# Optimization experiments

Measured on AMD Instinct MI355X. Metric: run time of the kernel, lower is better.

## Reference

```python
import jax, jax.numpy as jnp
import numpy as np

EMBED_DIM = 768
NUM_HEADS = 12
HEAD_DIM = EMBED_DIM // NUM_HEADS
SCALE = HEAD_DIM ** -0.5
EPS = 1e-5


def _layernorm(x, g, b):
    m = jnp.mean(x, axis=-1, keepdims=True)
    v = jnp.mean(jnp.square(x - m), axis=-1, keepdims=True)
    return (x - m) * jax.lax.rsqrt(v + EPS) * g + b


def setup_inputs() -> dict:
    key = jax.random.key(0)
    ks = jax.random.split(key, 8)
    B, N, D, Hd = 16, 1024, EMBED_DIM, HEAD_DIM
    x = jax.random.normal(ks[0], (B, N, D), dtype=jnp.float32)
    W_qkv = jax.random.normal(ks[1], (D, 3 * D), dtype=jnp.float32) * (D ** -0.5)
    b_qkv = jnp.zeros((3 * D,), dtype=jnp.float32)
    W_proj = jax.random.normal(ks[2], (D, D), dtype=jnp.float32) * (D ** -0.5)
    b_proj = jnp.zeros((D,), dtype=jnp.float32)
    return {
        "x": x,
        "ln_g": jnp.ones((D,), jnp.float32), "ln_b": jnp.zeros((D,), jnp.float32),
        "W_qkv": W_qkv, "b_qkv": b_qkv,
        "qn_g": jnp.ones((Hd,), jnp.float32), "qn_b": jnp.zeros((Hd,), jnp.float32),
        "kn_g": jnp.ones((Hd,), jnp.float32), "kn_b": jnp.zeros((Hd,), jnp.float32),
        "W_proj": W_proj, "b_proj": b_proj,
    }


def reference(x, ln_g, ln_b, W_qkv, b_qkv, qn_g, qn_b, kn_g, kn_b, W_proj, b_proj):
    B, N, D = x.shape
    H, Hd = NUM_HEADS, HEAD_DIM
    xn = _layernorm(x, ln_g, ln_b)                      # qkv_norm (pre-LN of embed_dim)
    qkv = xn @ W_qkv + b_qkv                            # [B,N,3D]
    qkv = qkv.reshape(B, N, 3, H, Hd)
    q = jnp.transpose(qkv[:, :, 0], (0, 2, 1, 3))       # [B,H,N,Hd]
    k = jnp.transpose(qkv[:, :, 1], (0, 2, 1, 3))
    v = jnp.transpose(qkv[:, :, 2], (0, 2, 1, 3))
    q = _layernorm(q, qn_g, qn_b)                       # per-head QK LayerNorm
    k = _layernorm(k, kn_g, kn_b)
    attn = jnp.einsum("bhnd,bhmd->bhnm", q, k) * SCALE
    attn = jax.nn.softmax(attn, axis=-1)
    out = jnp.einsum("bhnm,bhmd->bhnd", attn, v)        # [B,H,N,Hd]
    out = jnp.transpose(out, (0, 2, 1, 3)).reshape(B, N, D)
    return out @ W_proj + b_proj
```

## Files before the change

kernel.cpp:

```cpp
#include <hip/hip_runtime.h>

typedef _Float16 half8 __attribute__((ext_vector_type(8)));
typedef _Float16 half4 __attribute__((ext_vector_type(4)));
typedef _Float16 half2v __attribute__((ext_vector_type(2)));
typedef float f32x4 __attribute__((ext_vector_type(4)));

#define B_    16
#define N_    1024
#define D_    768
#define H_    12
#define M_    (B_ * N_)
#define QKVN_ 2304
#define EPS_  1e-5f
#define QS_   0.18033688011112042f

__device__ __forceinline__ float exp2_fast(float x) {
#if __has_builtin(__builtin_amdgcn_exp2f)
    return __builtin_amdgcn_exp2f(x);
#else
    return __builtin_exp2f(x);
#endif
}

__device__ __forceinline__ size_t aidx(int row, int d) {
    return ((size_t)((row >> 8) * 12 + (d >> 6))) * 16384
         + ((((row >> 4) & 15) * 2) + ((d >> 5) & 1)) * 512
         + (((d >> 3) & 3)) * 128 + (row & 15) * 8 + (d & 7);
}

__global__ __launch_bounds__(256) void convert_w(const float* __restrict__ Wqkv,
                                                 const float* __restrict__ Wproj,
                                                 _Float16* __restrict__ wqkv_p,
                                                 _Float16* __restrict__ wproj_p) {
    __shared__ float T[64][65];
    int t = blockIdx.x;
    const float* W; _Float16* O; int NW, k0, n0;
    if (t < 432) { W = Wqkv;  O = wqkv_p;  NW = QKVN_; k0 = (t % 12) * 64; n0 = (t / 12) * 64; }
    else { t -= 432; W = Wproj; O = wproj_p; NW = D_;  k0 = (t % 12) * 64; n0 = (t / 12) * 64; }
    int c = threadIdx.x & 63, r4 = threadIdx.x >> 6;
#pragma unroll
    for (int i = 0; i < 16; ++i) {
        int k = i * 4 + r4;
        T[c][k] = W[(size_t)(k0 + k) * NW + n0 + c];
    }
    __syncthreads();
    int kt = k0 >> 6;
    int ntile = n0 >> 7;
    int t16base = (n0 >> 4) & 7;
#pragma unroll
    for (int it = 0; it < 2; ++it) {
        int g = it * 256 + threadIdx.x;
        int t16l = g >> 7, ksub = (g >> 6) & 1, lgI = (g >> 4) & 3, p = g & 15;
        half8 v;
#pragma unroll
        for (int e = 0; e < 8; ++e)
            v[e] = (_Float16)T[t16l * 16 + p][ksub * 32 + lgI * 8 + e];
        *(half8*)&O[((size_t)(ntile * 12 + kt)) * 8192 +
                    ((t16base + t16l) * 2 + ksub) * 512 + lgI * 128 + p * 8] = v;
    }
}

__global__ __launch_bounds__(256) void ln_embed(const float* __restrict__ x,
                                                const float* __restrict__ g,
                                                const float* __restrict__ bb,
                                                _Float16* __restrict__ xp) {
    int row = blockIdx.x;
    int tid = threadIdx.x;
    const float2* xr = (const float2*)(x + (size_t)row * D_);
    float2 v0 = xr[tid];
    float2 v1 = make_float2(0.f, 0.f);
    if (tid < 128) v1 = xr[256 + tid];
    float s = v0.x + v0.y + v1.x + v1.y;
    float q = v0.x * v0.x + v0.y * v0.y + v1.x * v1.x + v1.y * v1.y;
#pragma unroll
    for (int m = 32; m >= 1; m >>= 1) {
        s += __shfl_xor(s, m);
        q += __shfl_xor(q, m);
    }
    __shared__ float ss[4], qq[4];
    int wave = tid >> 6;
    if ((tid & 63) == 0) { ss[wave] = s; qq[wave] = q; }
    __syncthreads();
    float S = ss[0] + ss[1] + ss[2] + ss[3];
    float Q = qq[0] + qq[1] + qq[2] + qq[3];
    float mean = S * (1.f / 768.f);
    float var  = Q * (1.f / 768.f) - mean * mean;
    float rstd = rsqrtf(var + EPS_);
    const float2* g2 = (const float2*)g;
    const float2* b2 = (const float2*)bb;
    {
        int d0 = 2 * tid;
        float2 ga = g2[tid], ba = b2[tid];
        half2v w;
        w[0] = (_Float16)((v0.x - mean) * rstd * ga.x + ba.x);
        w[1] = (_Float16)((v0.y - mean) * rstd * ga.y + ba.y);
        *(half2v*)&xp[aidx(row, d0)] = w;
    }
    if (tid < 128) {
        int d0 = 512 + 2 * tid;
        float2 ga = g2[256 + tid], ba = b2[256 + tid];
        half2v w;
        w[0] = (_Float16)((v1.x - mean) * rstd * ga.x + ba.x);
        w[1] = (_Float16)((v1.y - mean) * rstd * ga.y + ba.y);
        *(half2v*)&xp[aidx(row, d0)] = w;
    }
}

__global__ __launch_bounds__(256, 3) void gemm_qkv(const _Float16* __restrict__ Xp,
                                                   const _Float16* __restrict__ Wp,
                                                   const float* __restrict__ bias,
                                                   const float* __restrict__ qn_g,
                                                   const float* __restrict__ qn_b,
                                                   const float* __restrict__ kn_g,
                                                   const float* __restrict__ kn_b,
                                                   _Float16* __restrict__ qo,
                                                   _Float16* __restrict__ ko,
                                                   _Float16* __restrict__ vt) {
    int xcd = blockIdx.x & 7, loc = blockIdx.x >> 3;
    int mblk = xcd * 16 + (loc & 15);
    int nb = loc >> 4;
    int tid = threadIdx.x;
    int wid = tid >> 6, lane = tid & 63;
    int wm = wid >> 1, wn = wid & 1;
    int lg = lane >> 4, l15 = lane & 15;
    bool isV = (nb >= 12);

    const _Float16* pw = Wp + (size_t)nb * 98304 + (wn * 4) * 1024 + lane * 8;
    const _Float16* px = Xp + (size_t)(mblk >> 1) * 196608 +
                         ((mblk & 1) * 8 + wm * 4) * 1024 + lane * 8;

    f32x4 acc[4][4] = {};
    half8 xa0[4], wb0[4], xa1[4], wb1[4];
    auto ld = [&](half8 (&xa)[4], half8 (&wb)[4], int t) {
        int kt = t >> 1, ks = t & 1;
        size_t offW = (size_t)kt * 8192 + ks * 512;
        size_t offX = (size_t)kt * 16384 + ks * 512;
#pragma unroll
        for (int i = 0; i < 4; ++i) {
            xa[i] = *(const half8*)(px + i * 1024 + offX);
            wb[i] = *(const half8*)(pw + i * 1024 + offW);
        }
    };
    auto mmQK = [&](half8 (&xa)[4], half8 (&wb)[4]) {
#pragma unroll
        for (int ni = 0; ni < 4; ++ni)
#pragma unroll
            for (int mi = 0; mi < 4; ++mi)
                acc[ni][mi] = __builtin_amdgcn_mfma_f32_16x16x32_f16(wb[ni], xa[mi], acc[ni][mi], 0, 0, 0);
    };
    auto mmV = [&](half8 (&xa)[4], half8 (&wb)[4]) {
#pragma unroll
        for (int mi = 0; mi < 4; ++mi)
#pragma unroll
            for (int ni = 0; ni < 4; ++ni)
                acc[mi][ni] = __builtin_amdgcn_mfma_f32_16x16x32_f16(xa[mi], wb[ni], acc[mi][ni], 0, 0, 0);
    };

    ld(xa0, wb0, 0);
    if (isV) {
        for (int tt = 0; tt < 11; ++tt) {
            ld(xa1, wb1, 2 * tt + 1);
            mmV(xa0, wb0);
            ld(xa0, wb0, 2 * tt + 2);
            mmV(xa1, wb1);
        }
        ld(xa1, wb1, 23);
        mmV(xa0, wb0);
        mmV(xa1, wb1);
    } else {
        for (int tt = 0; tt < 11; ++tt) {
            ld(xa1, wb1, 2 * tt + 1);
            mmQK(xa0, wb0);
            ld(xa0, wb0, 2 * tt + 2);
            mmQK(xa1, wb1);
        }
        ld(xa1, wb1, 23);
        mmQK(xa0, wb0);
        mmQK(xa1, wb1);
    }

    int m0 = mblk * 128;
    int col0 = nb * 128 + wn * 64;

    if (isV) {
        int hcol = (col0 % 768) >> 6;
        float qkvb[4];
#pragma unroll
        for (int ni = 0; ni < 4; ++ni) qkvb[ni] = bias[col0 + ni * 16 + l15];
#pragma unroll
        for (int mi = 0; mi < 4; ++mi) {
            int r0 = m0 + wm * 64 + mi * 16 + lg * 4;
            int bidx = r0 >> 10, pos = r0 & 1023;
            int kvblk = pos >> 5, h = (pos >> 4) & 1, lgR = (pos >> 2) & 3;
            size_t vbase = ((size_t)(bidx * H_ + hcol) * 32 + kvblk) * 4;
#pragma unroll
            for (int ni = 0; ni < 4; ++ni) {
                half4 h4;
#pragma unroll
                for (int j = 0; j < 4; ++j) h4[j] = (_Float16)(acc[mi][ni][j] + qkvb[ni]);
                *(half4*)&vt[(vbase + ni) * 512 + lgR * 128 + l15 * 8 + h * 4] = h4;
            }
        }
    } else {
        int s = col0 / 768;
        int hcol = (col0 % 768) >> 6;
        const float* gg = (s == 0) ? qn_g : kn_g;
        const float* bv = (s == 0) ? qn_b : kn_b;
        _Float16* dst = (s == 0) ? qo : ko;
        float4 g4[4], b4[4], bi4[4];
#pragma unroll
        for (int ni = 0; ni < 4; ++ni) {
            g4[ni]  = *(const float4*)&gg[ni * 16 + lg * 4];
            b4[ni]  = *(const float4*)&bv[ni * 16 + lg * 4];
            bi4[ni] = *(const float4*)&bias[col0 + ni * 16 + lg * 4];
        }
        int posbase = m0 + wm * 64;
        int bidx = posbase >> 10;
        size_t bh0 = (size_t)(bidx * H_ + hcol) * 65536;
        float scl = (s == 0) ? QS_ : 1.0f;
#pragma unroll
        for (int mi = 0; mi < 4; ++mi) {
            float vv[4][4];
            float sm = 0.f, sq = 0.f;
#pragma unroll
            for (int ni = 0; ni < 4; ++ni)
#pragma unroll
                for (int j = 0; j < 4; ++j) {
                    float bvj = (j == 0) ? bi4[ni].x : (j == 1) ? bi4[ni].y : (j == 2) ? bi4[ni].z : bi4[ni].w;
                    float v = acc[ni][mi][j] + bvj;
                    vv[ni][j] = v;
                    sm += v;
                    sq += v * v;
                }
            sm += __shfl_xor(sm, 16); sq += __shfl_xor(sq, 16);
            sm += __shfl_xor(sm, 32); sq += __shfl_xor(sq, 32);
            float mean = sm * (1.f / 64.f);
            float var  = sq * (1.f / 64.f) - mean * mean;
            float rstd = rsqrtf(var + EPS_) * scl;
            float meanb = mean;
            int posL = ((posbase & 1023) + mi * 16);
            size_t obase = bh0 + (size_t)(posL >> 5) * 2048 + ((posL >> 4) & 1) * 1024
                         + l15 * 8 + (lg & 1) * 4;
#pragma unroll
            for (int ni = 0; ni < 4; ++ni) {
                half4 h4;
#pragma unroll
                for (int j = 0; j < 4; ++j) {
                    float gj = (j == 0) ? g4[ni].x : (j == 1) ? g4[ni].y : (j == 2) ? g4[ni].z : g4[ni].w;
                    float bj = (j == 0) ? b4[ni].x : (j == 1) ? b4[ni].y : (j == 2) ? b4[ni].z : b4[ni].w;
                    h4[j] = (_Float16)((vv[ni][j] - meanb) * rstd * gj + bj * scl);
                }
                dst[obase + (ni >> 1) * 512 + (((ni & 1) << 1) | (lg >> 1)) * 128] = h4[0];
                *(half4*)&dst[obase + (ni >> 1) * 512 + (((ni & 1) << 1) | (lg >> 1)) * 128] = h4;
            }
        }
    }
}

struct KV {
    half8 kf[2][2];
    half8 vf[4];
};

__device__ __forceinline__ void ldKV(KV& s, const _Float16* kp, const _Float16* vp, int kvblk) {
    const _Float16* kb = kp + (size_t)kvblk * 2048;
#pragma unroll
    for (int nh = 0; nh < 2; ++nh)
#pragma unroll
        for (int ks = 0; ks < 2; ++ks)
            s.kf[nh][ks] = *(const half8*)(kb + (nh * 2 + ks) * 512);
    const _Float16* vb = vp + (size_t)kvblk * 2048;
#pragma unroll
    for (int di = 0; di < 4; ++di)
        s.vf[di] = *(const half8*)(vb + di * 512);
}

__device__ __forceinline__ void blockKV(const KV& s, const half8 (&qf)[4][2],
                                        f32x4 (&oacc)[4][4], f32x4 (&lacc)[4],
                                        half8 ones) {
#pragma unroll
    for (int mi = 0; mi < 4; ++mi) {
        f32x4 a0 = {}, a1 = {};
#pragma unroll
        for (int ks = 0; ks < 2; ++ks) {
            a0 = __builtin_amdgcn_mfma_f32_16x16x32_f16(s.kf[0][ks], qf[mi][ks], a0, 0, 0, 0);
            a1 = __builtin_amdgcn_mfma_f32_16x16x32_f16(s.kf[1][ks], qf[mi][ks], a1, 0, 0, 0);
        }
        half8 pf;
#pragma unroll
        for (int j = 0; j < 4; ++j) {
            pf[j]     = (_Float16)exp2_fast(a0[j]);
            pf[j + 4] = (_Float16)exp2_fast(a1[j]);
        }
        lacc[mi] = __builtin_amdgcn_mfma_f32_16x16x32_f16(ones, pf, lacc[mi], 0, 0, 0);
#pragma unroll
        for (int di = 0; di < 4; ++di)
            oacc[mi][di] = __builtin_amdgcn_mfma_f32_16x16x32_f16(s.vf[di], pf, oacc[mi][di], 0, 0, 0);
    }
}

__global__ __launch_bounds__(128, 2) void attn(const _Float16* __restrict__ qg,
                                               const _Float16* __restrict__ kg,
                                               const _Float16* __restrict__ vtg,
                                               _Float16* __restrict__ op) {
    int bphys = blockIdx.x;
    int jj = (bphys & 7) * 192 + (bphys >> 3);
    int bh = jj >> 3, qt = jj & 7;
    int b = bh / H_, h = bh % H_;
    int tid = threadIdx.x;
    int wid = tid >> 6, lane = tid & 63;
    int lg = lane >> 4, l15 = lane & 15;
    int qw0 = qt * 128 + wid * 64;

    const _Float16* qp2 = qg + (size_t)bh * 65536 + (size_t)(qw0 >> 5) * 2048 + lane * 8;
    half8 qf[4][2];
#pragma unroll
    for (int mi = 0; mi < 4; ++mi)
#pragma unroll
        for (int ks = 0; ks < 2; ++ks)
            qf[mi][ks] = *(const half8*)(qp2 + (mi >> 1) * 2048 + (mi & 1) * 1024 + ks * 512);

    const _Float16* kp = kg + (size_t)bh * 65536 + lane * 8;
    const _Float16* vp = vtg + (size_t)bh * 65536 + lane * 8;

    half8 ones;
#pragma unroll
    for (int i = 0; i < 8; ++i) ones[i] = (_Float16)1.0f;

    f32x4 oacc[4][4] = {};
    f32x4 lacc[4] = {};

    KV s0, s1;
    ldKV(s0, kp, vp, 0);
    for (int t = 0; t < 16; ++t) {
        ldKV(s1, kp, vp, (2 * t + 1) & 31);
        blockKV(s0, qf, oacc, lacc, ones);
        ldKV(s0, kp, vp, (2 * t + 2) & 31);
        blockKV(s1, qf, oacc, lacc, ones);
    }

#pragma unroll
    for (int mi = 0; mi < 4; ++mi) {
        float inv = 1.f / lacc[mi][0];
        int row0 = b * 1024 + qw0 + mi * 16;
        int mtv = row0 >> 8, t16 = (row0 >> 4) & 15;
#pragma unroll
        for (int di = 0; di < 4; ++di) {
            half4 h4;
#pragma unroll
            for (int j = 0; j < 4; ++j) h4[j] = (_Float16)(oacc[mi][di][j] * inv);
            size_t o = ((size_t)(mtv * 12 + h)) * 16384 + (t16 * 2 + (di >> 1)) * 512
                     + ((di & 1) * 2 + (lg >> 1)) * 128 + l15 * 8 + (lg & 1) * 4;
            *(half4*)&op[o] = h4;
        }
    }
}

__global__ __launch_bounds__(256, 3) void gemm_proj(const _Float16* __restrict__ Ap,
                                                    const _Float16* __restrict__ Wp,
                                                    const float* __restrict__ bias,
                                                    float* __restrict__ out) {
    int xcd = blockIdx.x & 7, loc = blockIdx.x >> 3;
    int mblk = xcd * 16 + (loc & 15);
    int nb = loc >> 4;
    int tid = threadIdx.x;
    int wid = tid >> 6, lane = tid & 63;
    int wm = wid >> 1, wn = wid & 1;
    int lg = lane >> 4, l15 = lane & 15;

    const _Float16* pw = Wp + (size_t)nb * 98304 + (wn * 4) * 1024 + lane * 8;
    const _Float16* px = Ap + (size_t)(mblk >> 1) * 196608 +
                         ((mblk & 1) * 8 + wm * 4) * 1024 + lane * 8;

    f32x4 acc[4][4] = {};
    half8 xa0[4], wb0[4], xa1[4], wb1[4];
    auto ld = [&](half8 (&xa)[4], half8 (&wb)[4], int t) {
        int kt = t >> 1, ks = t & 1;
        size_t offW = (size_t)kt * 8192 + ks * 512;
        size_t offX = (size_t)kt * 16384 + ks * 512;
#pragma unroll
        for (int i = 0; i < 4; ++i) {
            xa[i] = *(const half8*)(px + i * 1024 + offX);
            wb[i] = *(const half8*)(pw + i * 1024 + offW);
        }
    };
    auto mm = [&](half8 (&xa)[4], half8 (&wb)[4]) {
#pragma unroll
        for (int mi = 0; mi < 4; ++mi)
#pragma unroll
            for (int ni = 0; ni < 4; ++ni)
                acc[mi][ni] = __builtin_amdgcn_mfma_f32_16x16x32_f16(xa[mi], wb[ni], acc[mi][ni], 0, 0, 0);
    };
    ld(xa0, wb0, 0);
    for (int tt = 0; tt < 11; ++tt) {
        ld(xa1, wb1, 2 * tt + 1);
        mm(xa0, wb0);
        ld(xa0, wb0, 2 * tt + 2);
        mm(xa1, wb1);
    }
    ld(xa1, wb1, 23);
    mm(xa0, wb0);
    mm(xa1, wb1);

    int m0 = mblk * 128, n0 = nb * 128;
#pragma unroll
    for (int mi = 0; mi < 4; ++mi)
#pragma unroll
        for (int ni = 0; ni < 4; ++ni) {
            int col = n0 + wn * 64 + ni * 16 + l15;
            float bv = bias[col];
#pragma unroll
            for (int j = 0; j < 4; ++j) {
                int row = m0 + wm * 64 + mi * 16 + lg * 4 + j;
                out[(size_t)row * D_ + col] = acc[mi][ni][j] + bv;
            }
        }
}

extern "C" void kernel_launch(void* const* d_in, const int* in_sizes, int n_in,
                              void* d_out, int out_size, void* d_ws, size_t ws_size,
                              hipStream_t stream) {
    const float* x      = (const float*)d_in[0];
    const float* ln_g   = (const float*)d_in[1];
    const float* ln_b   = (const float*)d_in[2];
    const float* W_qkv  = (const float*)d_in[3];
    const float* b_qkv  = (const float*)d_in[4];
    const float* qn_g   = (const float*)d_in[5];
    const float* qn_b   = (const float*)d_in[6];
    const float* kn_g   = (const float*)d_in[7];
    const float* kn_b   = (const float*)d_in[8];
    const float* W_proj = (const float*)d_in[9];
    const float* b_proj = (const float*)d_in[10];
    float* out = (float*)d_out;
    char* ws = (char*)d_ws;

    constexpr size_t XN_SZ    = (size_t)M_ * D_ * 2;
    constexpr size_t WQKVT_SZ = (size_t)QKVN_ * D_ * 2;
    constexpr size_t WPROJT_SZ= (size_t)D_ * D_ * 2;
    constexpr size_t HEAD_SZ  = (size_t)B_ * H_ * N_ * 64 * 2;

    _Float16* xn_p   = (_Float16*)(ws);
    _Float16* wqkv_p = (_Float16*)(ws + XN_SZ);
    _Float16* wproj_p= (_Float16*)(ws + XN_SZ + WQKVT_SZ);
    _Float16* qb     = (_Float16*)(ws + XN_SZ + WQKVT_SZ + WPROJT_SZ);
    _Float16* kb     = (_Float16*)((char*)qb + HEAD_SZ);
    _Float16* vtb    = (_Float16*)((char*)kb + HEAD_SZ);
    _Float16* ao_p   = xn_p;

    convert_w<<<576, 256, 0, stream>>>(W_qkv, W_proj, wqkv_p, wproj_p);
    ln_embed<<<M_, 256, 0, stream>>>(x, ln_g, ln_b, xn_p);
    gemm_qkv<<<(M_ / 128) * (QKVN_ / 128), 256, 0, stream>>>(xn_p, wqkv_p, b_qkv,
                                                             qn_g, qn_b, kn_g, kn_b,
                                                             qb, kb, vtb);
    attn<<<B_ * H_ * (N_ / 128), 128, 0, stream>>>(qb, kb, vtb, ao_p);
    gemm_proj<<<(M_ / 128) * (D_ / 128), 256, 0, stream>>>(ao_p, wproj_p, b_proj, out);
}
```

Before: 190.1 us.

## Split attention KV range across waves and merge prep kernels into one launch

Attention blocks now cover 64 query rows, with each of the two waves processing half of the KV sequence. The partial outputs and row sums are combined through shared memory, which doubles the grid and shortens each wave's serial loop. The weight conversion and embed LayerNorm kernels are merged into a single launch, and a redundant scalar store in the QKV epilogue is removed. The split adds a shared-memory reduction and a barrier, and leaves one wave idle during the epilogue.

```diff
diff --git a/kernel.cpp b/kernel.cpp
--- a/kernel.cpp
+++ b/kernel.cpp
@@ -28,81 +28,84 @@
          + (((d >> 3) & 3)) * 128 + (row & 15) * 8 + (d & 7);
 }
 
-__global__ __launch_bounds__(256) void convert_w(const float* __restrict__ Wqkv,
-                                                 const float* __restrict__ Wproj,
-                                                 _Float16* __restrict__ wqkv_p,
-                                                 _Float16* __restrict__ wproj_p) {
+__global__ __launch_bounds__(256) void prep(const float* __restrict__ x,
+                                            const float* __restrict__ ln_g,
+                                            const float* __restrict__ ln_b,
+                                            const float* __restrict__ Wqkv,
+                                            const float* __restrict__ Wproj,
+                                            _Float16* __restrict__ xp,
+                                            _Float16* __restrict__ wqkv_p,
+                                            _Float16* __restrict__ wproj_p) {
     __shared__ float T[64][65];
-    int t = blockIdx.x;
-    const float* W; _Float16* O; int NW, k0, n0;
-    if (t < 432) { W = Wqkv;  O = wqkv_p;  NW = QKVN_; k0 = (t % 12) * 64; n0 = (t / 12) * 64; }
-    else { t -= 432; W = Wproj; O = wproj_p; NW = D_;  k0 = (t % 12) * 64; n0 = (t / 12) * 64; }
-    int c = threadIdx.x & 63, r4 = threadIdx.x >> 6;
-#pragma unroll
-    for (int i = 0; i < 16; ++i) {
-        int k = i * 4 + r4;
-        T[c][k] = W[(size_t)(k0 + k) * NW + n0 + c];
-    }
-    __syncthreads();
-    int kt = k0 >> 6;
-    int ntile = n0 >> 7;
-    int t16base = (n0 >> 4) & 7;
-#pragma unroll
-    for (int it = 0; it < 2; ++it) {
-        int g = it * 256 + threadIdx.x;
-        int t16l = g >> 7, ksub = (g >> 6) & 1, lgI = (g >> 4) & 3, p = g & 15;
-        half8 v;
-#pragma unroll
-        for (int e = 0; e < 8; ++e)
-            v[e] = (_Float16)T[t16l * 16 + p][ksub * 32 + lgI * 8 + e];
-        *(half8*)&O[((size_t)(ntile * 12 + kt)) * 8192 +
-                    ((t16base + t16l) * 2 + ksub) * 512 + lgI * 128 + p * 8] = v;
-    }
-}
-
-__global__ __launch_bounds__(256) void ln_embed(const float* __restrict__ x,
-                                                const float* __restrict__ g,
-                                                const float* __restrict__ bb,
-                                                _Float16* __restrict__ xp) {
-    int row = blockIdx.x;
-    int tid = threadIdx.x;
-    const float2* xr = (const float2*)(x + (size_t)row * D_);
-    float2 v0 = xr[tid];
-    float2 v1 = make_float2(0.f, 0.f);
-    if (tid < 128) v1 = xr[256 + tid];
-    float s = v0.x + v0.y + v1.x + v1.y;
-    float q = v0.x * v0.x + v0.y * v0.y + v1.x * v1.x + v1.y * v1.y;
-#pragma unroll
-    for (int m = 32; m >= 1; m >>= 1) {
-        s += __shfl_xor(s, m);
-        q += __shfl_xor(q, m);
-    }
-    __shared__ float ss[4], qq[4];
-    int wave = tid >> 6;
-    if ((tid & 63) == 0) { ss[wave] = s; qq[wave] = q; }
-    __syncthreads();
-    float S = ss[0] + ss[1] + ss[2] + ss[3];
-    float Q = qq[0] + qq[1] + qq[2] + qq[3];
-    float mean = S * (1.f / 768.f);
-    float var  = Q * (1.f / 768.f) - mean * mean;
-    float rstd = rsqrtf(var + EPS_);
-    const float2* g2 = (const float2*)g;
-    const float2* b2 = (const float2*)bb;
-    {
-        int d0 = 2 * tid;
-        float2 ga = g2[tid], ba = b2[tid];
-        half2v w;
-        w[0] = (_Float16)((v0.x - mean) * rstd * ga.x + ba.x);
-        w[1] = (_Float16)((v0.y - mean) * rstd * ga.y + ba.y);
-        *(half2v*)&xp[aidx(row, d0)] = w;
-    }
-    if (tid < 128) {
-        int d0 = 512 + 2 * tid;
-        float2 ga = g2[256 + tid], ba = b2[256 + tid];
-        half2v w;
-        w[0] = (_Float16)((v1.x - mean) * rstd * ga.x + ba.x);
-        w[1] = (_Float16)((v1.y - mean) * rstd * ga.y + ba.y);
-        *(half2v*)&xp[aidx(row, d0)] = w;
+    int tb = blockIdx.x;
+    if (tb < 576) {
+        int t = tb;
+        const float* W; _Float16* O; int NW, k0, n0;
+        if (t < 432) { W = Wqkv;  O = wqkv_p;  NW = QKVN_; k0 = (t % 12) * 64; n0 = (t / 12) * 64; }
+        else { t -= 432; W = Wproj; O = wproj_p; NW = D_;  k0 = (t % 12) * 64; n0 = (t / 12) * 64; }
+        int c = threadIdx.x & 63, r4 = threadIdx.x >> 6;
+#pragma unroll
+        for (int i = 0; i < 16; ++i) {
+            int k = i * 4 + r4;
+            T[c][k] = W[(size_t)(k0 + k) * NW + n0 + c];
+        }
+        __syncthreads();
+        int kt = k0 >> 6;
+        int ntile = n0 >> 7;
+        int t16base = (n0 >> 4) & 7;
+#pragma unroll
+        for (int it = 0; it < 2; ++it) {
+            int g = it * 256 + threadIdx.x;
+            int t16l = g >> 7, ksub = (g >> 6) & 1, lgI = (g >> 4) & 3, p = g & 15;
+            half8 v;
+#pragma unroll
+            for (int e = 0; e < 8; ++e)
+                v[e] = (_Float16)T[t16l * 16 + p][ksub * 32 + lgI * 8 + e];
+            *(half8*)&O[((size_t)(ntile * 12 + kt)) * 8192 +
+                        ((t16base + t16l) * 2 + ksub) * 512 + lgI * 128 + p * 8] = v;
+        }
+    } else {
+        int row = tb - 576;
+        int tid = threadIdx.x;
+        const float2* xr = (const float2*)(x + (size_t)row * D_);
+        float2 v0 = xr[tid];
+        float2 v1 = make_float2(0.f, 0.f);
+        if (tid < 128) v1 = xr[256 + tid];
+        float s = v0.x + v0.y + v1.x + v1.y;
+        float q = v0.x * v0.x + v0.y * v0.y + v1.x * v1.x + v1.y * v1.y;
+#pragma unroll
+        for (int m = 32; m >= 1; m >>= 1) {
+            s += __shfl_xor(s, m);
+            q += __shfl_xor(q, m);
+        }
+        float* ss = &T[0][0];
+        float* qq = &T[0][8];
+        int wave = tid >> 6;
+        if ((tid & 63) == 0) { ss[wave] = s; qq[wave] = q; }
+        __syncthreads();
+        float S = ss[0] + ss[1] + ss[2] + ss[3];
+        float Q = qq[0] + qq[1] + qq[2] + qq[3];
+        float mean = S * (1.f / 768.f);
+        float var  = Q * (1.f / 768.f) - mean * mean;
+        float rstd = rsqrtf(var + EPS_);
+        const float2* g2 = (const float2*)ln_g;
+        const float2* b2 = (const float2*)ln_b;
+        {
+            int d0 = 2 * tid;
+            float2 ga = g2[tid], ba = b2[tid];
+            half2v w;
+            w[0] = (_Float16)((v0.x - mean) * rstd * ga.x + ba.x);
+            w[1] = (_Float16)((v0.y - mean) * rstd * ga.y + ba.y);
+            *(half2v*)&xp[aidx(row, d0)] = w;
+        }
+        if (tid < 128) {
+            int d0 = 512 + 2 * tid;
+            float2 ga = g2[256 + tid], ba = b2[256 + tid];
+            half2v w;
+            w[0] = (_Float16)((v1.x - mean) * rstd * ga.x + ba.x);
+            w[1] = (_Float16)((v1.y - mean) * rstd * ga.y + ba.y);
+            *(half2v*)&xp[aidx(row, d0)] = w;
+        }
     }
 }
 
@@ -237,7 +240,6 @@
             float mean = sm * (1.f / 64.f);
             float var  = sq * (1.f / 64.f) - mean * mean;
             float rstd = rsqrtf(var + EPS_) * scl;
-            float meanb = mean;
             int posL = ((posbase & 1023) + mi * 16);
             size_t obase = bh0 + (size_t)(posL >> 5) * 2048 + ((posL >> 4) & 1) * 1024
                          + l15 * 8 + (lg & 1) * 4;
@@ -248,9 +250,8 @@
                 for (int j = 0; j < 4; ++j) {
                     float gj = (j == 0) ? g4[ni].x : (j == 1) ? g4[ni].y : (j == 2) ? g4[ni].z : g4[ni].w;
                     float bj = (j == 0) ? b4[ni].x : (j == 1) ? b4[ni].y : (j == 2) ? b4[ni].z : b4[ni].w;
-                    h4[j] = (_Float16)((vv[ni][j] - meanb) * rstd * gj + bj * scl);
+                    h4[j] = (_Float16)((vv[ni][j] - mean) * rstd * gj + bj * scl);
                 }
-                dst[obase + (ni >> 1) * 512 + (((ni & 1) << 1) | (lg >> 1)) * 128] = h4[0];
                 *(half4*)&dst[obase + (ni >> 1) * 512 + (((ni & 1) << 1) | (lg >> 1)) * 128] = h4;
             }
         }
@@ -303,14 +304,16 @@
                                                const _Float16* __restrict__ kg,
                                                const _Float16* __restrict__ vtg,
                                                _Float16* __restrict__ op) {
+    __shared__ float OB[4][4][4][4][16];
+    __shared__ float LB[4][16];
     int bphys = blockIdx.x;
-    int jj = (bphys & 7) * 192 + (bphys >> 3);
-    int bh = jj >> 3, qt = jj & 7;
+    int jj = (bphys & 7) * 384 + (bphys >> 3);
+    int bh = jj >> 4, qgi = jj & 15;
     int b = bh / H_, h = bh % H_;
     int tid = threadIdx.x;
     int wid = tid >> 6, lane = tid & 63;
     int lg = lane >> 4, l15 = lane & 15;
-    int qw0 = qt * 128 + wid * 64;
+    int qw0 = qgi * 64;
 
     const _Float16* qp2 = qg + (size_t)bh * 65536 + (size_t)(qw0 >> 5) * 2048 + lane * 8;
     half8 qf[4][2];
@@ -322,6 +325,7 @@
 
     const _Float16* kp = kg + (size_t)bh * 65536 + lane * 8;
     const _Float16* vp = vtg + (size_t)bh * 65536 + lane * 8;
+    int kvbase = wid * 16;
 
     half8 ones;
 #pragma unroll
@@ -331,27 +335,42 @@
     f32x4 lacc[4] = {};
 
     KV s0, s1;
-    ldKV(s0, kp, vp, 0);
-    for (int t = 0; t < 16; ++t) {
-        ldKV(s1, kp, vp, (2 * t + 1) & 31);
+    ldKV(s0, kp, vp, kvbase);
+    for (int t = 0; t < 8; ++t) {
+        ldKV(s1, kp, vp, kvbase + ((2 * t + 1) & 15));
         blockKV(s0, qf, oacc, lacc, ones);
-        ldKV(s0, kp, vp, (2 * t + 2) & 31);
+        ldKV(s0, kp, vp, kvbase + ((2 * t + 2) & 15));
         blockKV(s1, qf, oacc, lacc, ones);
     }
 
-#pragma unroll
-    for (int mi = 0; mi < 4; ++mi) {
-        float inv = 1.f / lacc[mi][0];
-        int row0 = b * 1024 + qw0 + mi * 16;
-        int mtv = row0 >> 8, t16 = (row0 >> 4) & 15;
-#pragma unroll
-        for (int di = 0; di < 4; ++di) {
-            half4 h4;
-#pragma unroll
-            for (int j = 0; j < 4; ++j) h4[j] = (_Float16)(oacc[mi][di][j] * inv);
-            size_t o = ((size_t)(mtv * 12 + h)) * 16384 + (t16 * 2 + (di >> 1)) * 512
-                     + ((di & 1) * 2 + (lg >> 1)) * 128 + l15 * 8 + (lg & 1) * 4;
-            *(half4*)&op[o] = h4;
+    if (wid == 1) {
+#pragma unroll
+        for (int mi = 0; mi < 4; ++mi) {
+#pragma unroll
+            for (int di = 0; di < 4; ++di)
+#pragma unroll
+                for (int j = 0; j < 4; ++j)
+                    OB[mi][di][j][lg][l15] = oacc[mi][di][j];
+            if (lg == 0) LB[mi][l15] = lacc[mi][0];
+        }
+    }
+    __syncthreads();
+    if (wid == 0) {
+#pragma unroll
+        for (int mi = 0; mi < 4; ++mi) {
+            float inv = 1.f / (lacc[mi][0] + LB[mi][l15]);
+            int row0 = b * 1024 + qw0 + mi * 16;
+            int mtv = row0 >> 8, t16 = (row0 >> 4) & 15;
+#pragma unroll
+            for (int di = 0; di < 4; ++di) {
+                half4 h4;
+#pragma unroll
+                for (int j = 0; j < 4; ++j)
+                    h4[j] = (_Float16)((oacc[mi][di][j] + OB[mi][di][j][lg][l15]) * inv);
+                size_t o = ((size_t)(mtv * 12 + h)) * 16384 + (t16 * 2 + (di >> 1)) * 512
+                         + ((di & 1) * 2 + (lg >> 1)) * 128 + l15 * 8 + (lg & 1) * 4;
+                *(half4*)&op[o] = h4;
+            }
         }
     }
 }
@@ -447,11 +466,11 @@
     _Float16* vtb    = (_Float16*)((char*)kb + HEAD_SZ);
     _Float16* ao_p   = xn_p;
 
-    convert_w<<<576, 256, 0, stream>>>(W_qkv, W_proj, wqkv_p, wproj_p);
-    ln_embed<<<M_, 256, 0, stream>>>(x, ln_g, ln_b, xn_p);
+    prep<<<576 + M_, 256, 0, stream>>>(x, ln_g, ln_b, W_qkv, W_proj,
+                                       xn_p, wqkv_p, wproj_p);
     gemm_qkv<<<(M_ / 128) * (QKVN_ / 128), 256, 0, stream>>>(xn_p, wqkv_p, b_qkv,
                                                              qn_g, qn_b, kn_g, kn_b,
                                                              qb, kb, vtb);
-    attn<<<B_ * H_ * (N_ / 128), 128, 0, stream>>>(qb, kb, vtb, ao_p);
+    attn<<<B_ * H_ * (N_ / 64), 128, 0, stream>>>(qb, kb, vtb, ao_p);
     gemm_proj<<<(M_ / 128) * (D_ / 128), 256, 0, stream>>>(ao_p, wproj_p, b_proj, out);
 }
```

After: 189.6 us. About the same (-0.3%).
